# Kernel tuning notes

Hardware: AMD Instinct MI355X
Metric: run time of the kernel (lower is better)

The kernel has to match this reference:

```python
import jax, jax.numpy as jnp
import numpy as np

N, E = 50000, 800000
IN, HID, H, C = 128, 64, 4, 2
NEG_SLOPE = 0.2


def _gat_layer(h, src, dst, W, al, ar, b, out_dim, residual, resW=None, act='elu'):
    # h: [N, in]; W: [H*out, in]; al/ar: [H, out]; b: [H*out]
    n = h.shape[0]
    feat = (h @ W.T).reshape(n, H, out_dim)            # [N, H, out]
    el = jnp.einsum('nho,ho->nh', feat, al)            # [N, H]
    er = jnp.einsum('nho,ho->nh', feat, ar)            # [N, H]
    e = jax.nn.leaky_relu(el[src] + er[dst], NEG_SLOPE)  # [E, H]
    # segment softmax over incoming edges of each dst node
    emax = jax.ops.segment_max(e, dst, num_segments=n)
    ee = jnp.exp(e - emax[dst])
    denom = jax.ops.segment_sum(ee, dst, num_segments=n)
    alpha = ee / denom[dst]                             # [E, H]
    msg = feat[src] * alpha[:, :, None]                 # [E, H, out]
    rst = jax.ops.segment_sum(msg, dst, num_segments=n)  # [N, H, out]
    if residual == 'id':
        rst = rst + h.reshape(n, H, out_dim)
    elif residual == 'fc':
        rst = rst + (h @ resW.T).reshape(n, H, out_dim)
    rst = rst + b.reshape(1, H, out_dim)
    if act == 'elu':
        rst = jax.nn.elu(rst)
    else:  # softmax over last dim (F.softmax)
        rst = jax.nn.softmax(rst, axis=-1)
    return rst


def setup_inputs() -> dict:
    key = jax.random.key(0)
    ks = jax.random.split(key, 24)
    x = jax.random.normal(ks[0], (N, IN), dtype=jnp.float32)
    src = jax.random.randint(ks[1], (E,), 0, N)
    dst = jax.random.randint(ks[2], (E,), 0, N)
    s = 0.1
    d = {'x': x, 'src': src, 'dst': dst}
    # layer 1: IN -> (H, HID), no residual
    d['W1'] = jax.random.normal(ks[3], (H * HID, IN), dtype=jnp.float32) * s
    d['al1'] = jax.random.normal(ks[4], (H, HID), dtype=jnp.float32) * s
    d['ar1'] = jax.random.normal(ks[5], (H, HID), dtype=jnp.float32) * s
    d['b1'] = jnp.zeros((H * HID,), dtype=jnp.float32)
    # layers 2,3: H*HID -> (H, HID), identity residual
    d['W2'] = jax.random.normal(ks[6], (H * HID, H * HID), dtype=jnp.float32) * s
    d['al2'] = jax.random.normal(ks[7], (H, HID), dtype=jnp.float32) * s
    d['ar2'] = jax.random.normal(ks[8], (H, HID), dtype=jnp.float32) * s
    d['b2'] = jnp.zeros((H * HID,), dtype=jnp.float32)
    d['W3'] = jax.random.normal(ks[9], (H * HID, H * HID), dtype=jnp.float32) * s
    d['al3'] = jax.random.normal(ks[10], (H, HID), dtype=jnp.float32) * s
    d['ar3'] = jax.random.normal(ks[11], (H, HID), dtype=jnp.float32) * s
    d['b3'] = jnp.zeros((H * HID,), dtype=jnp.float32)
    # layer 4: H*HID -> (H, C), linear residual, softmax activation, mean over heads
    d['W4'] = jax.random.normal(ks[12], (H * C, H * HID), dtype=jnp.float32) * s
    d['al4'] = jax.random.normal(ks[13], (H, C), dtype=jnp.float32) * s
    d['ar4'] = jax.random.normal(ks[14], (H, C), dtype=jnp.float32) * s
    d['b4'] = jnp.zeros((H * C,), dtype=jnp.float32)
    d['resW4'] = jax.random.normal(ks[15], (H * C, H * HID), dtype=jnp.float32) * s
    return d


def reference(x, src, dst, W1, al1, ar1, b1, W2, al2, ar2, b2, W3, al3, ar3, b3, W4, al4, ar4, b4, resW4):
    h = _gat_layer(x, src, dst, W1, al1, ar1, b1, HID, 'none', act='elu').reshape(N, H * HID)
    h = _gat_layer(h, src, dst, W2, al2, ar2, b2, HID, 'id', act='elu').reshape(N, H * HID)
    h = _gat_layer(h, src, dst, W3, al3, ar3, b3, HID, 'id', act='elu').reshape(N, H * HID)
    h = _gat_layer(h, src, dst, W4, al4, ar4, b4, C, 'fc', resW=resW4, act='softmax')
    return h.mean(axis=1)  # [N, C]
```

## Files before the change

### kernel.cpp

```cpp
#include <hip/hip_runtime.h>
#include <hip/hip_bf16.h>
#include <math.h>


#define LEAKY_SLOPE 0.2f

typedef __bf16 bf16x8_t __attribute__((ext_vector_type(8)));
typedef float f32x4_t __attribute__((ext_vector_type(4)));

__device__ __forceinline__ float leaky(float x) { return x > 0.f ? x : LEAKY_SLOPE * x; }
__device__ __forceinline__ float eluf(float x)  { return x > 0.f ? x : expm1f(x); }
__device__ __forceinline__ float bflo(unsigned u) { return __uint_as_float(u << 16); }
__device__ __forceinline__ float bfhi(unsigned u) { return __uint_as_float(u & 0xffff0000u); }

__device__ __forceinline__ int rli(int v, int l) { return __builtin_amdgcn_readlane(v, l); }
__device__ __forceinline__ float rlf(float v, int l) {
  return __uint_as_float((unsigned)__builtin_amdgcn_readlane((int)__float_as_uint(v), l));
}
template <int CTRL>
__device__ __forceinline__ float dpp_add(float x) {
  int t = __builtin_amdgcn_update_dpp(0, (int)__float_as_uint(x), CTRL, 0xf, 0xf, false);
  return x + __uint_as_float((unsigned)t);
}
__device__ __forceinline__ float wsum_dpp(float x) {
  x = dpp_add<0x111>(x);
  x = dpp_add<0x112>(x);
  x = dpp_add<0x114>(x);
  x = dpp_add<0x118>(x);
  x = dpp_add<0x142>(x);
  x = dpp_add<0x143>(x);
  return rlf(x, 63);
}
__device__ __forceinline__ float wmax(float v) {
#pragma unroll
  for (int o = 32; o; o >>= 1) v = fmaxf(v, __shfl_xor(v, o));
  return v;
}
__device__ __forceinline__ float wsum_sh(float v) {
#pragma unroll
  for (int o = 32; o; o >>= 1) v += __shfl_xor(v, o);
  return v;
}

__global__ void hist_k(const int* __restrict__ dst, int* __restrict__ deg, int e) {
  int i = blockIdx.x * 256 + threadIdx.x;
  if (i < e) atomicAdd(&deg[dst[i]], 1);
}

__global__ __launch_bounds__(1024) void scan1_k(const int* __restrict__ deg,
                                                int* __restrict__ rowp,
                                                int* __restrict__ bsum, int n) {
  __shared__ int sd[1024];
  int tid = threadIdx.x;
  int i = blockIdx.x * 1024 + tid;
  int v = (i < n) ? deg[i] : 0;
  int x = v;
  sd[tid] = x;
  __syncthreads();
  for (int off = 1; off < 1024; off <<= 1) {
    int t = (tid >= off) ? sd[tid - off] : 0;
    __syncthreads();
    x += t;
    sd[tid] = x;
    __syncthreads();
  }
  if (i < n) rowp[i] = x - v;
  if (tid == 1023) bsum[blockIdx.x] = x;
}

__global__ __launch_bounds__(64) void scan2_k(int* __restrict__ bsum, int nb) {
  int lane = threadIdx.x;
  if (nb <= 64) {
    int v = (lane < nb) ? bsum[lane] : 0;
    int x = v;
#pragma unroll
    for (int off = 1; off < 64; off <<= 1) {
      int t = __shfl_up(x, off);
      if (lane >= off) x += t;
    }
    if (lane < nb) bsum[lane] = x - v;
    if (lane == 63) bsum[nb] = x;
  } else if (lane == 0) {
    int run = 0;
    for (int i = 0; i < nb; ++i) { int t = bsum[i]; bsum[i] = run; run += t; }
    bsum[nb] = run;
  }
}

__global__ void scan3_k(const int* __restrict__ bsum, int* __restrict__ rowp, int n, int nb) {
  int i = blockIdx.x * 256 + threadIdx.x;
  if (i < n) rowp[i] += bsum[i >> 10];
  if (i == n) rowp[n] = bsum[nb];
}

__global__ void scatter_k(const int* __restrict__ src, const int* __restrict__ dst,
                          const int* __restrict__ rowp, int* __restrict__ cur,
                          int* __restrict__ csrc, int e) {
  int i = blockIdx.x * 256 + threadIdx.x;
  if (i < e) {
    int d = dst[i];
    int p = atomicAdd(&cur[d], 1);
    csrc[rowp[d] + p] = src[i];
  }
}

__global__ void cvtall_k(const float* __restrict__ x, const float* __restrict__ W1,
                         const float* __restrict__ W2, const float* __restrict__ W3,
                         const float* __restrict__ W4, const float* __restrict__ rW4,
                         __hip_bfloat16* __restrict__ xb, __hip_bfloat16* __restrict__ W1b,
                         __hip_bfloat16* __restrict__ W2b, __hip_bfloat16* __restrict__ W3b,
                         __hip_bfloat16* __restrict__ Wcatb, int nx) {
  int i = blockIdx.x * 256 + threadIdx.x;
  if (i < nx) { xb[i] = __float2bfloat16(x[i]); return; }
  int j = i - nx;
  if (j < 32768) W1b[j] = __float2bfloat16(W1[j]);
  else if (j < 98304)  { int k = j - 32768;  W2b[k] = __float2bfloat16(W2[k]); }
  else if (j < 163840) { int k = j - 98304;  W3b[k] = __float2bfloat16(W3[k]); }
  else if (j < 165888) { int k = j - 163840; Wcatb[k] = __float2bfloat16(W4[k]); }
  else if (j < 167936) { int k = j - 165888; Wcatb[2048 + k] = __float2bfloat16(rW4[k]); }
}

template <int K>
__global__ __launch_bounds__(256) void gemm_mfma(const __hip_bfloat16* __restrict__ A,
                                                 const __hip_bfloat16* __restrict__ B,
                                                 __hip_bfloat16* __restrict__ featb,
                                                 const float* __restrict__ al,
                                                 const float* __restrict__ ar,
                                                 float* __restrict__ el,
                                                 float* __restrict__ er, int n) {
  __shared__ __bf16 As[128 * 40];
  __shared__ __bf16 Bs[128 * 40];
  const int tid = threadIdx.x;
  const int lane = tid & 63, w = tid >> 6;
  const int tm = lane & 15, tq = lane >> 4;
  const int wm = (w & 1) * 64, wn = (w >> 1) * 64;
  const int r0 = blockIdx.x * 128, c0 = blockIdx.y * 128;
  const int srow = tid >> 1, sko = (tid & 1) * 16;

  f32x4_t acc[4][4];
#pragma unroll
  for (int i = 0; i < 4; ++i)
#pragma unroll
    for (int j = 0; j < 4; ++j) acc[i][j] = 0.f;

  for (int kk = 0; kk < K; kk += 32) {
    uint4 av0 = {0, 0, 0, 0}, av1 = {0, 0, 0, 0};
    int arw = r0 + srow;
    if (arw < n) {
      const uint4* p = (const uint4*)(A + (size_t)arw * K + kk + sko);
      av0 = p[0];
      av1 = p[1];
    }
    const uint4* q = (const uint4*)(B + (size_t)(c0 + srow) * K + kk + sko);
    uint4 bv0 = q[0], bv1 = q[1];
    __syncthreads();
    *(uint4*)&As[srow * 40 + sko] = av0;
    *(uint4*)&As[srow * 40 + sko + 8] = av1;
    *(uint4*)&Bs[srow * 40 + sko] = bv0;
    *(uint4*)&Bs[srow * 40 + sko + 8] = bv1;
    __syncthreads();
    bf16x8_t af[4], bfr[4];
#pragma unroll
    for (int i = 0; i < 4; ++i) af[i] = *(const bf16x8_t*)&As[(wm + i * 16 + tm) * 40 + tq * 8];
#pragma unroll
    for (int j = 0; j < 4; ++j) bfr[j] = *(const bf16x8_t*)&Bs[(wn + j * 16 + tm) * 40 + tq * 8];
#pragma unroll
    for (int i = 0; i < 4; ++i)
#pragma unroll
      for (int j = 0; j < 4; ++j)
        acc[i][j] = __builtin_amdgcn_mfma_f32_16x16x32_bf16(af[i], bfr[j], acc[i][j], 0, 0, 0);
  }

#pragma unroll
  for (int i = 0; i < 4; ++i) {
#pragma unroll
    for (int j = 0; j < 4; ++j) {
      int col = c0 + wn + j * 16 + tm;
      int hh = col >> 6, oo = col & 63;
#pragma unroll
      for (int rr = 0; rr < 4; ++rr) {
        int row = r0 + wm + i * 16 + tq * 4 + rr;
        if (row < n) featb[(size_t)row * 256 + oo * 4 + hh] = __float2bfloat16(acc[i][j][rr]);
      }
    }
  }

  {
    const int hd = (c0 + wn) >> 6;
    float alv[4], arv[4];
#pragma unroll
    for (int j = 0; j < 4; ++j) {
      alv[j] = al[hd * 64 + j * 16 + tm];
      arv[j] = ar[hd * 64 + j * 16 + tm];
    }
#pragma unroll
    for (int i = 0; i < 4; ++i) {
#pragma unroll
      for (int rr = 0; rr < 4; ++rr) {
        float se = acc[i][0][rr] * alv[0] + acc[i][1][rr] * alv[1] +
                   acc[i][2][rr] * alv[2] + acc[i][3][rr] * alv[3];
        float sr2 = acc[i][0][rr] * arv[0] + acc[i][1][rr] * arv[1] +
                    acc[i][2][rr] * arv[2] + acc[i][3][rr] * arv[3];
#pragma unroll
        for (int o = 1; o < 16; o <<= 1) {
          se += __shfl_xor(se, o);
          sr2 += __shfl_xor(sr2, o);
        }
        if (tm == 0) {
          int row = r0 + wm + i * 16 + tq * 4 + rr;
          if (row < n) {
            el[(size_t)row * 4 + hd] = se;
            er[(size_t)row * 4 + hd] = sr2;
          }
        }
      }
    }
  }
}

template <int RES>
__global__ __launch_bounds__(256) void agg64_k(const __hip_bfloat16* __restrict__ featb,
                                               const float* __restrict__ el,
                                               const float* __restrict__ er,
                                               const int* __restrict__ rowp,
                                               const int* __restrict__ csrc,
                                               const __hip_bfloat16* __restrict__ hinb,
                                               const float* __restrict__ bias,
                                               __hip_bfloat16* __restrict__ houtb, int n) {
  __shared__ float wsh[4][256];
  int wv = threadIdx.x >> 6;
  int node = blockIdx.x * 4 + wv;
  int lane = threadIdx.x & 63;
  if (node >= n) return;
  int s0 = rowp[node], s1 = rowp[node + 1];
  int deg = s1 - s0;
  float4 erv = *(const float4*)(er + (size_t)node * 4);
  float a0 = 0, a1 = 0, a2 = 0, a3 = 0;
  float i0 = 1.f, i1 = 1.f, i2 = 1.f, i3 = 1.f;

  if (deg <= 64) {
    int sown = 0;
    float x0 = 0.f, x1 = 0.f, x2 = 0.f, x3 = 0.f;
    if (lane < deg) {
      sown = csrc[s0 + lane];
      float4 e = *(const float4*)(el + (size_t)sown * 4);
      x0 = __expf(leaky(e.x + erv.x));
      x1 = __expf(leaky(e.y + erv.y));
      x2 = __expf(leaky(e.z + erv.z));
      x3 = __expf(leaky(e.w + erv.w));
    }
    float d0 = wsum_dpp(x0), d1 = wsum_dpp(x1), d2 = wsum_dpp(x2), d3 = wsum_dpp(x3);
    i0 = d0 > 0.f ? 1.f / d0 : 0.f;
    i1 = d1 > 0.f ? 1.f / d1 : 0.f;
    i2 = d2 > 0.f ? 1.f / d2 : 0.f;
    i3 = d3 > 0.f ? 1.f / d3 : 0.f;

    float4 wq = {x0, x1, x2, x3};
    *(float4*)&wsh[wv][lane * 4] = wq;

    int k = 0;
    for (; k + 4 <= deg; k += 4) {
      int sk0 = rli(sown, k + 0), sk1 = rli(sown, k + 1);
      int sk2 = rli(sown, k + 2), sk3 = rli(sown, k + 3);
      uint2 u0 = ((const uint2*)(featb + ((size_t)sk0 << 8)))[lane];
      uint2 u1 = ((const uint2*)(featb + ((size_t)sk1 << 8)))[lane];
      uint2 u2 = ((const uint2*)(featb + ((size_t)sk2 << 8)))[lane];
      uint2 u3 = ((const uint2*)(featb + ((size_t)sk3 << 8)))[lane];
      float4 w0 = *(const float4*)&wsh[wv][(k + 0) * 4];
      float4 w1 = *(const float4*)&wsh[wv][(k + 1) * 4];
      float4 w2 = *(const float4*)&wsh[wv][(k + 2) * 4];
      float4 w3 = *(const float4*)&wsh[wv][(k + 3) * 4];
      a0 = fmaf(w0.x, bflo(u0.x), a0); a1 = fmaf(w0.y, bfhi(u0.x), a1);
      a2 = fmaf(w0.z, bflo(u0.y), a2); a3 = fmaf(w0.w, bfhi(u0.y), a3);
      a0 = fmaf(w1.x, bflo(u1.x), a0); a1 = fmaf(w1.y, bfhi(u1.x), a1);
      a2 = fmaf(w1.z, bflo(u1.y), a2); a3 = fmaf(w1.w, bfhi(u1.y), a3);
      a0 = fmaf(w2.x, bflo(u2.x), a0); a1 = fmaf(w2.y, bfhi(u2.x), a1);
      a2 = fmaf(w2.z, bflo(u2.y), a2); a3 = fmaf(w2.w, bfhi(u2.y), a3);
      a0 = fmaf(w3.x, bflo(u3.x), a0); a1 = fmaf(w3.y, bfhi(u3.x), a1);
      a2 = fmaf(w3.z, bflo(u3.y), a2); a3 = fmaf(w3.w, bfhi(u3.y), a3);
    }
    for (; k < deg; ++k) {
      int sk = rli(sown, k);
      uint2 u = ((const uint2*)(featb + ((size_t)sk << 8)))[lane];
      float4 wk = *(const float4*)&wsh[wv][k * 4];
      a0 = fmaf(wk.x, bflo(u.x), a0);
      a1 = fmaf(wk.y, bfhi(u.x), a1);
      a2 = fmaf(wk.z, bflo(u.y), a2);
      a3 = fmaf(wk.w, bfhi(u.y), a3);
    }
  } else {
    float m0 = -INFINITY, m1 = -INFINITY, m2 = -INFINITY, m3 = -INFINITY;
    for (int k = s0 + lane; k < s1; k += 64) {
      int s = csrc[k];
      float4 e = *(const float4*)(el + (size_t)s * 4);
      m0 = fmaxf(m0, leaky(e.x + erv.x));
      m1 = fmaxf(m1, leaky(e.y + erv.y));
      m2 = fmaxf(m2, leaky(e.z + erv.z));
      m3 = fmaxf(m3, leaky(e.w + erv.w));
    }
    m0 = wmax(m0); m1 = wmax(m1); m2 = wmax(m2); m3 = wmax(m3);
    float d0 = 0, d1 = 0, d2 = 0, d3 = 0;
    for (int k = s0 + lane; k < s1; k += 64) {
      int s = csrc[k];
      float4 e = *(const float4*)(el + (size_t)s * 4);
      d0 += __expf(leaky(e.x + erv.x) - m0);
      d1 += __expf(leaky(e.y + erv.y) - m1);
      d2 += __expf(leaky(e.z + erv.z) - m2);
      d3 += __expf(leaky(e.w + erv.w) - m3);
    }
    d0 = wsum_sh(d0); d1 = wsum_sh(d1); d2 = wsum_sh(d2); d3 = wsum_sh(d3);
    float j0 = d0 > 0.f ? 1.f / d0 : 0.f;
    float j1 = d1 > 0.f ? 1.f / d1 : 0.f;
    float j2 = d2 > 0.f ? 1.f / d2 : 0.f;
    float j3 = d3 > 0.f ? 1.f / d3 : 0.f;
    for (int k = s0; k < s1; ++k) {
      int s = csrc[k];
      float4 e = *(const float4*)(el + (size_t)s * 4);
      float w0 = __expf(leaky(e.x + erv.x) - m0) * j0;
      float w1 = __expf(leaky(e.y + erv.y) - m1) * j1;
      float w2 = __expf(leaky(e.z + erv.z) - m2) * j2;
      float w3 = __expf(leaky(e.w + erv.w) - m3) * j3;
      uint2 u = ((const uint2*)(featb + ((size_t)s << 8)))[lane];
      a0 = fmaf(w0, bflo(u.x), a0);
      a1 = fmaf(w1, bfhi(u.x), a1);
      a2 = fmaf(w2, bflo(u.y), a2);
      a3 = fmaf(w3, bfhi(u.y), a3);
    }
  }

  size_t base = (size_t)node * 256;
  float v0 = a0 * i0 + bias[lane];
  float v1 = a1 * i1 + bias[64 + lane];
  float v2 = a2 * i2 + bias[128 + lane];
  float v3 = a3 * i3 + bias[192 + lane];
  if (RES) {
    v0 += __bfloat162float(hinb[base + lane]);
    v1 += __bfloat162float(hinb[base + 64 + lane]);
    v2 += __bfloat162float(hinb[base + 128 + lane]);
    v3 += __bfloat162float(hinb[base + 192 + lane]);
  }
  houtb[base + lane]       = __float2bfloat16(eluf(v0));
  houtb[base + 64 + lane]  = __float2bfloat16(eluf(v1));
  houtb[base + 128 + lane] = __float2bfloat16(eluf(v2));
  houtb[base + 192 + lane] = __float2bfloat16(eluf(v3));
}

__global__ __launch_bounds__(256) void l4mfma_k(const __hip_bfloat16* __restrict__ hb,
                                                const __hip_bfloat16* __restrict__ Wcat,
                                                const float* __restrict__ al4,
                                                const float* __restrict__ ar4,
                                                float* __restrict__ feat4,
                                                float* __restrict__ res4,
                                                float* __restrict__ el4,
                                                float* __restrict__ er4, int n) {
  int wid = blockIdx.x * 4 + (threadIdx.x >> 6);
  int n16 = (n + 15) >> 4;
  if (wid >= n16) return;
  int lane = threadIdx.x & 63;
  int tm = lane & 15, tq = lane >> 4;
  int row = wid * 16 + tm;
  int rowc = row < n ? row : n - 1;
  const __hip_bfloat16* ap = hb + (size_t)rowc * 256 + tq * 8;
  const __hip_bfloat16* bp = Wcat + (size_t)tm * 256 + tq * 8;
  f32x4_t acc = {0.f, 0.f, 0.f, 0.f};
#pragma unroll
  for (int k = 0; k < 8; ++k) {
    bf16x8_t af = *(const bf16x8_t*)(ap + k * 32);
    bf16x8_t bf = *(const bf16x8_t*)(bp + k * 32);
    acc = __builtin_amdgcn_mfma_f32_16x16x32_bf16(af, bf, acc, 0, 0, 0);
  }
  float* dstp = (tm < 8) ? feat4 : res4;
  int cc = tm & 7;
  float a4 = (tm < 8) ? al4[tm] : 0.f;
  float r4 = (tm < 8) ? ar4[tm] : 0.f;
#pragma unroll
  for (int r = 0; r < 4; ++r) {
    int node = wid * 16 + tq * 4 + r;
    float te = acc[r] * a4;
    float tr = acc[r] * r4;
    te += __shfl_xor(te, 1);
    tr += __shfl_xor(tr, 1);
    if (node < n) {
      dstp[(size_t)node * 8 + cc] = acc[r];
      if (tm < 8 && (tm & 1) == 0) {
        el4[(size_t)node * 4 + (tm >> 1)] = te;
        er4[(size_t)node * 4 + (tm >> 1)] = tr;
      }
    }
  }
}

__global__ __launch_bounds__(256) void agg4_k(const float* __restrict__ feat4,
                                              const float* __restrict__ el4,
                                              const float* __restrict__ er4,
                                              const int* __restrict__ rowp,
                                              const int* __restrict__ csrc,
                                              const float* __restrict__ res4,
                                              const float* __restrict__ b4,
                                              float* __restrict__ out, int n) {
  __shared__ int ssh[4][64];
  __shared__ float wsh[4][256];
  int wv = threadIdx.x >> 6;
  int node = blockIdx.x * 4 + wv;
  int lane = threadIdx.x & 63;
  if (node >= n) return;
  int s0 = rowp[node], s1 = rowp[node + 1];
  int deg = s1 - s0;
  float4 erv = *(const float4*)(er4 + (size_t)node * 4);
  float acc = 0.f;
  float scale = 1.f;
  int p = lane & 7, hh = p >> 1;

  if (deg <= 64) {
    int sown = 0;
    float x0 = 0.f, x1 = 0.f, x2 = 0.f, x3 = 0.f;
    if (lane < deg) {
      sown = csrc[s0 + lane];
      float4 e = *(const float4*)(el4 + (size_t)sown * 4);
      x0 = __expf(leaky(e.x + erv.x));
      x1 = __expf(leaky(e.y + erv.y));
      x2 = __expf(leaky(e.z + erv.z));
      x3 = __expf(leaky(e.w + erv.w));
    }
    float d0 = wsum_dpp(x0), d1 = wsum_dpp(x1), d2 = wsum_dpp(x2), d3 = wsum_dpp(x3);
    float i0 = d0 > 0.f ? 1.f / d0 : 0.f;
    float i1 = d1 > 0.f ? 1.f / d1 : 0.f;
    float i2 = d2 > 0.f ? 1.f / d2 : 0.f;
    float i3 = d3 > 0.f ? 1.f / d3 : 0.f;
    scale = (hh == 0) ? i0 : (hh == 1) ? i1 : (hh == 2) ? i2 : i3;
    ssh[wv][lane] = sown;
    float4 wq = {x0, x1, x2, x3};
    *(float4*)&wsh[wv][lane * 4] = wq;
    int g = lane >> 3;
    int nt = (deg + 7) >> 3;
    for (int t = 0; t < nt; ++t) {
      int k = g + t * 8;
      bool ok = k < deg;
      int kk = k & 63;
      int sk = ssh[wv][kk];
      float wk = wsh[wv][kk * 4 + hh];
      if (ok) acc = fmaf(wk, feat4[(size_t)sk * 8 + p], acc);
    }
    acc += __shfl_xor(acc, 8);
    acc += __shfl_xor(acc, 16);
    acc += __shfl_xor(acc, 32);
  } else {
    float m0 = -INFINITY, m1 = -INFINITY, m2 = -INFINITY, m3 = -INFINITY;
    for (int k = s0 + lane; k < s1; k += 64) {
      int s = csrc[k];
      float4 e = *(const float4*)(el4 + (size_t)s * 4);
      m0 = fmaxf(m0, leaky(e.x + erv.x));
      m1 = fmaxf(m1, leaky(e.y + erv.y));
      m2 = fmaxf(m2, leaky(e.z + erv.z));
      m3 = fmaxf(m3, leaky(e.w + erv.w));
    }
    m0 = wmax(m0); m1 = wmax(m1); m2 = wmax(m2); m3 = wmax(m3);
    float d0 = 0, d1 = 0, d2 = 0, d3 = 0;
    for (int k = s0 + lane; k < s1; k += 64) {
      int s = csrc[k];
      float4 e = *(const float4*)(el4 + (size_t)s * 4);
      d0 += __expf(leaky(e.x + erv.x) - m0);
      d1 += __expf(leaky(e.y + erv.y) - m1);
      d2 += __expf(leaky(e.z + erv.z) - m2);
      d3 += __expf(leaky(e.w + erv.w) - m3);
    }
    d0 = wsum_sh(d0); d1 = wsum_sh(d1); d2 = wsum_sh(d2); d3 = wsum_sh(d3);
    float i0 = d0 > 0.f ? 1.f / d0 : 0.f;
    float i1 = d1 > 0.f ? 1.f / d1 : 0.f;
    float i2 = d2 > 0.f ? 1.f / d2 : 0.f;
    float i3 = d3 > 0.f ? 1.f / d3 : 0.f;
    for (int k = s0; k < s1; ++k) {
      int s = csrc[k];
      float4 e = *(const float4*)(el4 + (size_t)s * 4);
      float w0 = __expf(leaky(e.x + erv.x) - m0) * i0;
      float w1 = __expf(leaky(e.y + erv.y) - m1) * i1;
      float w2 = __expf(leaky(e.z + erv.z) - m2) * i2;
      float w3 = __expf(leaky(e.w + erv.w) - m3) * i3;
      float wk = (hh == 0) ? w0 : (hh == 1) ? w1 : (hh == 2) ? w2 : w3;
      if (lane < 8) acc = fmaf(wk, feat4[(size_t)s * 8 + p], acc);
    }
  }

  float v = 0.f;
  if (lane < 8) v = acc * scale + res4[(size_t)node * 8 + lane] + b4[lane];
  float pv = __shfl_xor(v, 1);
  float mx = fmaxf(v, pv);
  float ex = __expf(v - mx);
  float sm = ex + __shfl_xor(ex, 1);
  float pr = ex / sm;
  float t = pr + __shfl_xor(pr, 2);
  t += __shfl_xor(t, 4);
  if (lane < 2) out[(size_t)node * 2 + lane] = t * 0.25f;
}

extern "C" void kernel_launch(void* const* d_in, const int* in_sizes, int n_in,
                              void* d_out, int out_size, void* d_ws, size_t ws_size,
                              hipStream_t stream) {
  const float* x   = (const float*)d_in[0];
  const int* src   = (const int*)d_in[1];
  const int* dst   = (const int*)d_in[2];
  const float* W1  = (const float*)d_in[3];
  const float* al1 = (const float*)d_in[4];
  const float* ar1 = (const float*)d_in[5];
  const float* b1  = (const float*)d_in[6];
  const float* W2  = (const float*)d_in[7];
  const float* al2 = (const float*)d_in[8];
  const float* ar2 = (const float*)d_in[9];
  const float* b2  = (const float*)d_in[10];
  const float* W3  = (const float*)d_in[11];
  const float* al3 = (const float*)d_in[12];
  const float* ar3 = (const float*)d_in[13];
  const float* b3  = (const float*)d_in[14];
  const float* W4  = (const float*)d_in[15];
  const float* al4 = (const float*)d_in[16];
  const float* ar4 = (const float*)d_in[17];
  const float* b4  = (const float*)d_in[18];
  const float* rW4 = (const float*)d_in[19];
  float* out = (float*)d_out;

  const int n = in_sizes[0] / 128;
  const int e = in_sizes[1];

  char* ws = (char*)d_ws;
  auto alloc = [&](size_t bytes) -> char* {
    char* p = ws;
    ws += (bytes + 255) & ~(size_t)255;
    return p;
  };
  __hip_bfloat16* featb = (__hip_bfloat16*)alloc((size_t)n * 256 * 2);
  __hip_bfloat16* h1b   = (__hip_bfloat16*)alloc((size_t)n * 256 * 2);
  __hip_bfloat16* h2b   = (__hip_bfloat16*)alloc((size_t)n * 256 * 2);
  __hip_bfloat16* h3b   = (__hip_bfloat16*)alloc((size_t)n * 256 * 2);
  __hip_bfloat16* xb    = (__hip_bfloat16*)alloc((size_t)n * 128 * 2);
  __hip_bfloat16* W1b   = (__hip_bfloat16*)alloc((size_t)256 * 128 * 2);
  __hip_bfloat16* W2b   = (__hip_bfloat16*)alloc((size_t)256 * 256 * 2);
  __hip_bfloat16* W3b   = (__hip_bfloat16*)alloc((size_t)256 * 256 * 2);
  __hip_bfloat16* Wcatb = (__hip_bfloat16*)alloc((size_t)16 * 256 * 2);
  float* el    = (float*)alloc((size_t)n * 4 * 4);
  float* er    = (float*)alloc((size_t)n * 4 * 4);
  float* feat4 = (float*)alloc((size_t)n * 8 * 4);
  float* res4  = (float*)alloc((size_t)n * 8 * 4);
  float* el4   = (float*)alloc((size_t)n * 4 * 4);
  float* er4   = (float*)alloc((size_t)n * 4 * 4);
  int* deg     = (int*)alloc((size_t)n * 4);
  int* cur     = (int*)alloc((size_t)n * 4);
  int* rowp    = (int*)alloc((size_t)(n + 1) * 4);
  int* csrc    = (int*)alloc((size_t)e * 4);
  int nb_scan  = (n + 1023) / 1024;
  int* bsum    = (int*)alloc((size_t)(nb_scan + 1) * 4);

  (void)hipMemsetAsync(deg, 0, (size_t)n * 4, stream);
  (void)hipMemsetAsync(cur, 0, (size_t)n * 4, stream);
  hist_k<<<(e + 255) / 256, 256, 0, stream>>>(dst, deg, e);
  scan1_k<<<nb_scan, 1024, 0, stream>>>(deg, rowp, bsum, n);
  scan2_k<<<1, 64, 0, stream>>>(bsum, nb_scan);
  scan3_k<<<(n + 256) / 256, 256, 0, stream>>>(bsum, rowp, n, nb_scan);
  scatter_k<<<(e + 255) / 256, 256, 0, stream>>>(src, dst, rowp, cur, csrc, e);

  int nx = n * 128;
  cvtall_k<<<(nx + 167936 + 255) / 256, 256, 0, stream>>>(x, W1, W2, W3, W4, rW4, xb, W1b,
                                                          W2b, W3b, Wcatb, nx);

  dim3 ggrid((n + 127) / 128, 2);
  int nb4 = (n + 3) / 4;

  gemm_mfma<128><<<ggrid, 256, 0, stream>>>(xb, W1b, featb, al1, ar1, el, er, n);
  agg64_k<0><<<nb4, 256, 0, stream>>>(featb, el, er, rowp, csrc, nullptr, b1, h1b, n);
  gemm_mfma<256><<<ggrid, 256, 0, stream>>>(h1b, W2b, featb, al2, ar2, el, er, n);
  agg64_k<1><<<nb4, 256, 0, stream>>>(featb, el, er, rowp, csrc, h1b, b2, h2b, n);
  gemm_mfma<256><<<ggrid, 256, 0, stream>>>(h2b, W3b, featb, al3, ar3, el, er, n);
  agg64_k<1><<<nb4, 256, 0, stream>>>(featb, el, er, rowp, csrc, h2b, b3, h3b, n);
  int n16 = (n + 15) / 16;
  l4mfma_k<<<(n16 + 3) / 4, 256, 0, stream>>>(h3b, Wcatb, al4, ar4, feat4, res4, el4, er4, n);
  agg4_k<<<nb4, 256, 0, stream>>>(feat4, el4, er4, rowp, csrc, res4, b4, out, n);
}
```

Before: 515.7 us.

## Use direct global-to-LDS loads in GEMM and unroll aggregation gather by eight

For interior tiles, the GEMM now stages A and B through global_load_lds, which writes straight into unpadded LDS tiles and skips the register round-trip. Boundary tiles keep the old register path, now also with the 32-wide stride. The aggregation kernel folds the softmax normalisation into the shared edge weights and adds an 8-way unrolled gather loop, so more feature loads are in flight per wave. Dropping the LDS padding can add bank conflicts on the MFMA fragment reads, and the larger unroll raises register pressure.

```diff
diff --git a/kernel.cpp b/kernel.cpp
--- a/kernel.cpp
+++ b/kernel.cpp
@@ -40,6 +40,11 @@
 #pragma unroll
   for (int o = 32; o; o >>= 1) v += __shfl_xor(v, o);
   return v;
+}
+
+__device__ __forceinline__ void gl_lds16(const __hip_bfloat16* g, __bf16* l) {
+  __builtin_amdgcn_global_load_lds((const __attribute__((address_space(1))) void*)g,
+                                   (__attribute__((address_space(3))) void*)l, 16, 0, 0);
 }
 
 __global__ void hist_k(const int* __restrict__ dst, int* __restrict__ deg, int e) {
@@ -128,14 +133,13 @@
                                                  const float* __restrict__ ar,
                                                  float* __restrict__ el,
                                                  float* __restrict__ er, int n) {
-  __shared__ __bf16 As[128 * 40];
-  __shared__ __bf16 Bs[128 * 40];
+  __shared__ __bf16 As[128 * 32];
+  __shared__ __bf16 Bs[128 * 32];
   const int tid = threadIdx.x;
   const int lane = tid & 63, w = tid >> 6;
   const int tm = lane & 15, tq = lane >> 4;
   const int wm = (w & 1) * 64, wn = (w >> 1) * 64;
   const int r0 = blockIdx.x * 128, c0 = blockIdx.y * 128;
-  const int srow = tid >> 1, sko = (tid & 1) * 16;
 
   f32x4_t acc[4][4];
 #pragma unroll
@@ -143,32 +147,59 @@
 #pragma unroll
     for (int j = 0; j < 4; ++j) acc[i][j] = 0.f;
 
-  for (int kk = 0; kk < K; kk += 32) {
-    uint4 av0 = {0, 0, 0, 0}, av1 = {0, 0, 0, 0};
-    int arw = r0 + srow;
-    if (arw < n) {
-      const uint4* p = (const uint4*)(A + (size_t)arw * K + kk + sko);
-      av0 = p[0];
-      av1 = p[1];
-    }
-    const uint4* q = (const uint4*)(B + (size_t)(c0 + srow) * K + kk + sko);
-    uint4 bv0 = q[0], bv1 = q[1];
-    __syncthreads();
-    *(uint4*)&As[srow * 40 + sko] = av0;
-    *(uint4*)&As[srow * 40 + sko + 8] = av1;
-    *(uint4*)&Bs[srow * 40 + sko] = bv0;
-    *(uint4*)&Bs[srow * 40 + sko + 8] = bv1;
-    __syncthreads();
-    bf16x8_t af[4], bfr[4];
-#pragma unroll
-    for (int i = 0; i < 4; ++i) af[i] = *(const bf16x8_t*)&As[(wm + i * 16 + tm) * 40 + tq * 8];
-#pragma unroll
-    for (int j = 0; j < 4; ++j) bfr[j] = *(const bf16x8_t*)&Bs[(wn + j * 16 + tm) * 40 + tq * 8];
-#pragma unroll
-    for (int i = 0; i < 4; ++i)
-#pragma unroll
-      for (int j = 0; j < 4; ++j)
-        acc[i][j] = __builtin_amdgcn_mfma_f32_16x16x32_bf16(af[i], bfr[j], acc[i][j], 0, 0, 0);
+  const bool interior = (r0 + 128 <= n);
+  if (interior) {
+    const int srow = w * 32 + (lane >> 2);
+    const int scol = (lane & 3) * 8;
+    for (int kk = 0; kk < K; kk += 32) {
+      __syncthreads();
+      const __hip_bfloat16* ga = A + (size_t)(r0 + srow) * K + kk + scol;
+      const __hip_bfloat16* gb = B + (size_t)(c0 + srow) * K + kk + scol;
+      gl_lds16(ga, As + w * 1024);
+      gl_lds16(ga + (size_t)16 * K, As + w * 1024 + 512);
+      gl_lds16(gb, Bs + w * 1024);
+      gl_lds16(gb + (size_t)16 * K, Bs + w * 1024 + 512);
+      __syncthreads();
+      bf16x8_t af[4], bfr[4];
+#pragma unroll
+      for (int i = 0; i < 4; ++i) af[i] = *(const bf16x8_t*)&As[(wm + i * 16 + tm) * 32 + tq * 8];
+#pragma unroll
+      for (int j = 0; j < 4; ++j) bfr[j] = *(const bf16x8_t*)&Bs[(wn + j * 16 + tm) * 32 + tq * 8];
+#pragma unroll
+      for (int i = 0; i < 4; ++i)
+#pragma unroll
+        for (int j = 0; j < 4; ++j)
+          acc[i][j] = __builtin_amdgcn_mfma_f32_16x16x32_bf16(af[i], bfr[j], acc[i][j], 0, 0, 0);
+    }
+  } else {
+    const int srow = tid >> 1, sko = (tid & 1) * 16;
+    for (int kk = 0; kk < K; kk += 32) {
+      uint4 av0 = {0, 0, 0, 0}, av1 = {0, 0, 0, 0};
+      int arw = r0 + srow;
+      if (arw < n) {
+        const uint4* p = (const uint4*)(A + (size_t)arw * K + kk + sko);
+        av0 = p[0];
+        av1 = p[1];
+      }
+      const uint4* q = (const uint4*)(B + (size_t)(c0 + srow) * K + kk + sko);
+      uint4 bv0 = q[0], bv1 = q[1];
+      __syncthreads();
+      *(uint4*)&As[srow * 32 + sko] = av0;
+      *(uint4*)&As[srow * 32 + sko + 8] = av1;
+      *(uint4*)&Bs[srow * 32 + sko] = bv0;
+      *(uint4*)&Bs[srow * 32 + sko + 8] = bv1;
+      __syncthreads();
+      bf16x8_t af[4], bfr[4];
+#pragma unroll
+      for (int i = 0; i < 4; ++i) af[i] = *(const bf16x8_t*)&As[(wm + i * 16 + tm) * 32 + tq * 8];
+#pragma unroll
+      for (int j = 0; j < 4; ++j) bfr[j] = *(const bf16x8_t*)&Bs[(wn + j * 16 + tm) * 32 + tq * 8];
+#pragma unroll
+      for (int i = 0; i < 4; ++i)
+#pragma unroll
+        for (int j = 0; j < 4; ++j)
+          acc[i][j] = __builtin_amdgcn_mfma_f32_16x16x32_bf16(af[i], bfr[j], acc[i][j], 0, 0, 0);
+    }
   }
 
 #pragma unroll
@@ -236,7 +267,6 @@
   int deg = s1 - s0;
   float4 erv = *(const float4*)(er + (size_t)node * 4);
   float a0 = 0, a1 = 0, a2 = 0, a3 = 0;
-  float i0 = 1.f, i1 = 1.f, i2 = 1.f, i3 = 1.f;
 
   if (deg <= 64) {
     int sown = 0;
@@ -250,15 +280,52 @@
       x3 = __expf(leaky(e.w + erv.w));
     }
     float d0 = wsum_dpp(x0), d1 = wsum_dpp(x1), d2 = wsum_dpp(x2), d3 = wsum_dpp(x3);
-    i0 = d0 > 0.f ? 1.f / d0 : 0.f;
-    i1 = d1 > 0.f ? 1.f / d1 : 0.f;
-    i2 = d2 > 0.f ? 1.f / d2 : 0.f;
-    i3 = d3 > 0.f ? 1.f / d3 : 0.f;
-
-    float4 wq = {x0, x1, x2, x3};
+    float i0 = d0 > 0.f ? 1.f / d0 : 0.f;
+    float i1 = d1 > 0.f ? 1.f / d1 : 0.f;
+    float i2 = d2 > 0.f ? 1.f / d2 : 0.f;
+    float i3 = d3 > 0.f ? 1.f / d3 : 0.f;
+    float4 wq = {x0 * i0, x1 * i1, x2 * i2, x3 * i3};
     *(float4*)&wsh[wv][lane * 4] = wq;
 
     int k = 0;
+    for (; k + 8 <= deg; k += 8) {
+      int sk0 = rli(sown, k + 0), sk1 = rli(sown, k + 1);
+      int sk2 = rli(sown, k + 2), sk3 = rli(sown, k + 3);
+      int sk4 = rli(sown, k + 4), sk5 = rli(sown, k + 5);
+      int sk6 = rli(sown, k + 6), sk7 = rli(sown, k + 7);
+      uint2 u0 = ((const uint2*)(featb + ((size_t)sk0 << 8)))[lane];
+      uint2 u1 = ((const uint2*)(featb + ((size_t)sk1 << 8)))[lane];
+      uint2 u2 = ((const uint2*)(featb + ((size_t)sk2 << 8)))[lane];
+      uint2 u3 = ((const uint2*)(featb + ((size_t)sk3 << 8)))[lane];
+      uint2 u4 = ((const uint2*)(featb + ((size_t)sk4 << 8)))[lane];
+      uint2 u5 = ((const uint2*)(featb + ((size_t)sk5 << 8)))[lane];
+      uint2 u6 = ((const uint2*)(featb + ((size_t)sk6 << 8)))[lane];
+      uint2 u7 = ((const uint2*)(featb + ((size_t)sk7 << 8)))[lane];
+      float4 w0 = *(const float4*)&wsh[wv][(k + 0) * 4];
+      float4 w1 = *(const float4*)&wsh[wv][(k + 1) * 4];
+      float4 w2 = *(const float4*)&wsh[wv][(k + 2) * 4];
+      float4 w3 = *(const float4*)&wsh[wv][(k + 3) * 4];
+      float4 w4 = *(const float4*)&wsh[wv][(k + 4) * 4];
+      float4 w5 = *(const float4*)&wsh[wv][(k + 5) * 4];
+      float4 w6 = *(const float4*)&wsh[wv][(k + 6) * 4];
+      float4 w7 = *(const float4*)&wsh[wv][(k + 7) * 4];
+      a0 = fmaf(w0.x, bflo(u0.x), a0); a1 = fmaf(w0.y, bfhi(u0.x), a1);
+      a2 = fmaf(w0.z, bflo(u0.y), a2); a3 = fmaf(w0.w, bfhi(u0.y), a3);
+      a0 = fmaf(w1.x, bflo(u1.x), a0); a1 = fmaf(w1.y, bfhi(u1.x), a1);
+      a2 = fmaf(w1.z, bflo(u1.y), a2); a3 = fmaf(w1.w, bfhi(u1.y), a3);
+      a0 = fmaf(w2.x, bflo(u2.x), a0); a1 = fmaf(w2.y, bfhi(u2.x), a1);
+      a2 = fmaf(w2.z, bflo(u2.y), a2); a3 = fmaf(w2.w, bfhi(u2.y), a3);
+      a0 = fmaf(w3.x, bflo(u3.x), a0); a1 = fmaf(w3.y, bfhi(u3.x), a1);
+      a2 = fmaf(w3.z, bflo(u3.y), a2); a3 = fmaf(w3.w, bfhi(u3.y), a3);
+      a0 = fmaf(w4.x, bflo(u4.x), a0); a1 = fmaf(w4.y, bfhi(u4.x), a1);
+      a2 = fmaf(w4.z, bflo(u4.y), a2); a3 = fmaf(w4.w, bfhi(u4.y), a3);
+      a0 = fmaf(w5.x, bflo(u5.x), a0); a1 = fmaf(w5.y, bfhi(u5.x), a1);
+      a2 = fmaf(w5.z, bflo(u5.y), a2); a3 = fmaf(w5.w, bfhi(u5.y), a3);
+      a0 = fmaf(w6.x, bflo(u6.x), a0); a1 = fmaf(w6.y, bfhi(u6.x), a1);
+      a2 = fmaf(w6.z, bflo(u6.y), a2); a3 = fmaf(w6.w, bfhi(u6.y), a3);
+      a0 = fmaf(w7.x, bflo(u7.x), a0); a1 = fmaf(w7.y, bfhi(u7.x), a1);
+      a2 = fmaf(w7.z, bflo(u7.y), a2); a3 = fmaf(w7.w, bfhi(u7.y), a3);
+    }
     for (; k + 4 <= deg; k += 4) {
       int sk0 = rli(sown, k + 0), sk1 = rli(sown, k + 1);
       int sk2 = rli(sown, k + 2), sk3 = rli(sown, k + 3);
@@ -329,10 +396,10 @@
   }
 
   size_t base = (size_t)node * 256;
-  float v0 = a0 * i0 + bias[lane];
-  float v1 = a1 * i1 + bias[64 + lane];
-  float v2 = a2 * i2 + bias[128 + lane];
-  float v3 = a3 * i3 + bias[192 + lane];
+  float v0 = a0 + bias[lane];
+  float v1 = a1 + bias[64 + lane];
+  float v2 = a2 + bias[128 + lane];
+  float v3 = a3 + bias[192 + lane];
   if (RES) {
     v0 += __bfloat162float(hinb[base + lane]);
     v1 += __bfloat162float(hinb[base + 64 + lane]);
```

Result: no change. 508.7 us (-1.4%).
